# Performance work log

Hardware: AMD Instinct MI355X
Metric: run time of the kernel (lower is better)

Reference implementation:

```python
import jax, jax.numpy as jnp
import numpy as np

D_MODEL = 1024
NUM_HEADS = 16
HEAD_DIM = D_MODEL // NUM_HEADS
D_FF = 4096
BATCH = 4
SEQ = 2048
LN_EPS = 1e-6
NEG_INF = -1e10


def setup_inputs() -> dict:
    key = jax.random.key(0)
    ks = jax.random.split(key, 8)
    def lin_init(k, fan_in, fan_out):
        # flax default: lecun_normal kernel, zeros bias
        w = jax.random.normal(k, (fan_in, fan_out), jnp.float32) / np.sqrt(fan_in)
        b = jnp.zeros((fan_out,), jnp.float32)
        return w, b
    x = jax.random.normal(ks[0], (BATCH, SEQ, D_MODEL), jnp.float32)
    w_qkv, b_qkv = lin_init(ks[1], D_MODEL, 3 * D_MODEL)
    w_out, b_out = lin_init(ks[2], D_MODEL, D_MODEL)
    w_fc1, b_fc1 = lin_init(ks[3], D_MODEL, D_FF)
    w_fc2, b_fc2 = lin_init(ks[4], D_FF, D_MODEL)
    ln1_scale = jnp.ones((D_MODEL,), jnp.float32)
    ln1_bias = jnp.zeros((D_MODEL,), jnp.float32)
    ln2_scale = jnp.ones((D_MODEL,), jnp.float32)
    ln2_bias = jnp.zeros((D_MODEL,), jnp.float32)
    return {
        'x': x,
        'w_qkv': w_qkv, 'b_qkv': b_qkv,
        'w_out': w_out, 'b_out': b_out,
        'w_fc1': w_fc1, 'b_fc1': b_fc1,
        'w_fc2': w_fc2, 'b_fc2': b_fc2,
        'ln1_scale': ln1_scale, 'ln1_bias': ln1_bias,
        'ln2_scale': ln2_scale, 'ln2_bias': ln2_bias,
    }


def _layernorm(x, scale, bias):
    mu = jnp.mean(x, axis=-1, keepdims=True)
    var = jnp.mean(jnp.square(x - mu), axis=-1, keepdims=True)
    return (x - mu) * jax.lax.rsqrt(var + LN_EPS) * scale + bias


def _attention(x, w_qkv, b_qkv, w_out, b_out):
    B, S, _ = x.shape
    qkv = x @ w_qkv + b_qkv                      # [B,S,3*D]
    qkv = qkv.reshape(B, S, 3, NUM_HEADS, HEAD_DIM)
    q, k, v = qkv[:, :, 0], qkv[:, :, 1], qkv[:, :, 2]   # [B,S,H,D]
    q = q.transpose(0, 2, 1, 3)                  # [B,H,S,D]
    k = k.transpose(0, 2, 1, 3)
    v = v.transpose(0, 2, 1, 3)
    scores = jnp.einsum('bhqd,bhkd->bhqk', q, k) / np.sqrt(HEAD_DIM)
    causal = jnp.tril(jnp.ones((S, S), bool))[None, None]
    scores = jnp.where(causal, scores, NEG_INF)
    attn = jax.nn.softmax(scores, axis=-1)
    out = jnp.einsum('bhqk,bhkd->bhqd', attn, v)  # [B,H,S,D]
    out = out.transpose(0, 2, 1, 3).reshape(B, S, D_MODEL)
    return out @ w_out + b_out


def _mlp(x, w_fc1, b_fc1, w_fc2, b_fc2):
    h = jax.nn.gelu(x @ w_fc1 + b_fc1)  # approximate (tanh) gelu, matching nnx.gelu default
    return h @ w_fc2 + b_fc2


def reference(x, w_qkv, b_qkv, w_out, b_out, w_fc1, b_fc1, w_fc2, b_fc2,
              ln1_scale, ln1_bias, ln2_scale, ln2_bias):
    x = x + _attention(_layernorm(x, ln1_scale, ln1_bias), w_qkv, b_qkv, w_out, b_out)
    x = x + _mlp(_layernorm(x, ln2_scale, ln2_bias), w_fc1, b_fc1, w_fc2, b_fc2)
    return x
```

## Files before the change

### kernel.cpp

```cpp
#include <hip/hip_runtime.h>

typedef unsigned short u16;
typedef unsigned int u32;
typedef __bf16 bf16x8 __attribute__((ext_vector_type(8)));
typedef float f32x4 __attribute__((ext_vector_type(4)));

constexpr int SEQ = 2048;

__device__ __forceinline__ float bf2f(u16 u) {
    u32 x = ((u32)u) << 16;
    return __builtin_bit_cast(float, x);
}
__device__ __forceinline__ u16 f2bf(float f) {
    u32 u = __builtin_bit_cast(u32, f);
    u32 r = u + 0x7fffu + ((u >> 16) & 1u);
    return (u16)(r >> 16);
}
__device__ __forceinline__ bf16x8 ld_frag(const u16* p) {
    uint4 u = *(const uint4*)p;
    return __builtin_bit_cast(bf16x8, u);
}
__device__ __forceinline__ float gelu_f(float x) {
    float u = 0.7978845608028654f * (x + 0.044715f * x * x * x);
    float e = exp2f(u * 2.885390081777927f);
    float t = 1.f - 2.f / (1.f + e);
    return 0.5f * x * (1.f + t);
}
__device__ __forceinline__ bool probe_f32(const u32* p) { return (p[0] & 0xFFFFu) == 0u; }

__device__ __forceinline__ void load_lds16(const u16* g, u16* l) {
    __builtin_amdgcn_global_load_lds(
        (const __attribute__((address_space(1))) void*)g,
        (__attribute__((address_space(3))) void*)l, 16, 0, 0);
}

__global__ __launch_bounds__(256) void convert_to_bf16(const void* __restrict__ in, long long off,
                                                       u16* __restrict__ out, int n,
                                                       const u32* __restrict__ probe) {
    const bool f32 = probe_f32(probe);
    int i = (blockIdx.x * 256 + threadIdx.x) * 4;
    if (i >= n) return;
    if (f32) {
        const float4 v = *(const float4*)((const float*)in + off + i);
        uint2 o;
        o.x = (u32)f2bf(v.x) | ((u32)f2bf(v.y) << 16);
        o.y = (u32)f2bf(v.z) | ((u32)f2bf(v.w) << 16);
        *(uint2*)(out + i) = o;
    } else {
        *(uint2*)(out + i) = *(const uint2*)((const u16*)in + off + i);
    }
}

__global__ __launch_bounds__(256) void finalize_out(const u16* __restrict__ in, void* __restrict__ outv,
                                                    long long off, int n, const u32* __restrict__ probe) {
    const bool f32 = probe_f32(probe);
    int i = (blockIdx.x * 256 + threadIdx.x) * 4;
    if (i >= n) return;
    uint2 v = *(const uint2*)(in + i);
    if (f32) {
        float4 o;
        o.x = bf2f((u16)(v.x & 0xffffu));
        o.y = bf2f((u16)(v.x >> 16));
        o.z = bf2f((u16)(v.y & 0xffffu));
        o.w = bf2f((u16)(v.y >> 16));
        *(float4*)((float*)outv + off + i) = o;
    } else {
        *(uint2*)((u16*)outv + off + i) = v;
    }
}

__global__ __launch_bounds__(256) void transpose_any(const void* __restrict__ in,
                                                     u16* __restrict__ out,
                                                     int K, int N, const u32* __restrict__ probe) {
    const bool f32 = probe_f32(probe);
    __shared__ u16 tile[32][33];
    int tx = threadIdx.x & 31, ty = threadIdx.x >> 5;
    int k0 = blockIdx.y * 32, n0 = blockIdx.x * 32;
    for (int i = 0; i < 32; i += 8) {
        size_t idx = (size_t)(k0 + ty + i) * N + n0 + tx;
        tile[ty + i][tx] = f32 ? f2bf(((const float*)in)[idx]) : ((const u16*)in)[idx];
    }
    __syncthreads();
    for (int i = 0; i < 32; i += 8)
        out[(size_t)(n0 + ty + i) * K + k0 + tx] = tile[tx][ty + i];
}

__global__ __launch_bounds__(256) void fused_cvt_ln(const void* __restrict__ xraw, long long off,
                                                    const u16* __restrict__ sc,
                                                    const u16* __restrict__ bi,
                                                    u16* __restrict__ xbf,
                                                    u16* __restrict__ xn,
                                                    const u32* __restrict__ probe) {
    const bool f32 = probe_f32(probe);
    int row = blockIdx.x;
    int tid = threadIdx.x;
    float v[4];
    if (f32) {
        const float4 q = *(const float4*)((const float*)xraw + off + (size_t)row * 1024 + tid * 4);
        v[0] = q.x; v[1] = q.y; v[2] = q.z; v[3] = q.w;
    } else {
        uint2 u = *(const uint2*)((const u16*)xraw + off + (size_t)row * 1024 + tid * 4);
        v[0] = bf2f((u16)(u.x & 0xffffu)); v[1] = bf2f((u16)(u.x >> 16));
        v[2] = bf2f((u16)(u.y & 0xffffu)); v[3] = bf2f((u16)(u.y >> 16));
    }
    {
        uint2 c;
        c.x = (u32)f2bf(v[0]) | ((u32)f2bf(v[1]) << 16);
        c.y = (u32)f2bf(v[2]) | ((u32)f2bf(v[3]) << 16);
        *(uint2*)(xbf + (size_t)row * 1024 + tid * 4) = c;
    }
    float s1 = 0.f, s2 = 0.f;
    for (int i = 0; i < 4; i++) { s1 += v[i]; s2 += v[i] * v[i]; }
    for (int off2 = 32; off2 >= 1; off2 >>= 1) {
        s1 += __shfl_xor(s1, off2, 64);
        s2 += __shfl_xor(s2, off2, 64);
    }
    __shared__ float red[8];
    int wave = tid >> 6, lane = tid & 63;
    if (lane == 0) { red[wave] = s1; red[4 + wave] = s2; }
    __syncthreads();
    s1 = red[0] + red[1] + red[2] + red[3];
    s2 = red[4] + red[5] + red[6] + red[7];
    float mean = s1 * (1.f / 1024.f);
    float var = s2 * (1.f / 1024.f) - mean * mean;
    float rstd = rsqrtf(var + 1e-6f);
    int c = tid * 4;
    float y0 = (v[0] - mean) * rstd * bf2f(sc[c + 0]) + bf2f(bi[c + 0]);
    float y1 = (v[1] - mean) * rstd * bf2f(sc[c + 1]) + bf2f(bi[c + 1]);
    float y2 = (v[2] - mean) * rstd * bf2f(sc[c + 2]) + bf2f(bi[c + 2]);
    float y3 = (v[3] - mean) * rstd * bf2f(sc[c + 3]) + bf2f(bi[c + 3]);
    uint2 ov;
    ov.x = (u32)f2bf(y0) | ((u32)f2bf(y1) << 16);
    ov.y = (u32)f2bf(y2) | ((u32)f2bf(y3) << 16);
    *(uint2*)(xn + (size_t)row * 1024 + tid * 4) = ov;
}

__global__ __launch_bounds__(256) void layernorm_k(const u16* __restrict__ x,
                                                   const u16* __restrict__ sc,
                                                   const u16* __restrict__ bi,
                                                   u16* __restrict__ out) {
    int row = blockIdx.x;
    int tid = threadIdx.x;
    const u16* xr = x + (size_t)row * 1024;
    uint2 u = *(const uint2*)(xr + tid * 4);
    float v[4];
    v[0] = bf2f((u16)(u.x & 0xffffu));
    v[1] = bf2f((u16)(u.x >> 16));
    v[2] = bf2f((u16)(u.y & 0xffffu));
    v[3] = bf2f((u16)(u.y >> 16));
    float s1 = 0.f, s2 = 0.f;
    for (int i = 0; i < 4; i++) { s1 += v[i]; s2 += v[i] * v[i]; }
    for (int off = 32; off >= 1; off >>= 1) {
        s1 += __shfl_xor(s1, off, 64);
        s2 += __shfl_xor(s2, off, 64);
    }
    __shared__ float red[8];
    int wave = tid >> 6, lane = tid & 63;
    if (lane == 0) { red[wave] = s1; red[4 + wave] = s2; }
    __syncthreads();
    s1 = red[0] + red[1] + red[2] + red[3];
    s2 = red[4] + red[5] + red[6] + red[7];
    float mean = s1 * (1.f / 1024.f);
    float var = s2 * (1.f / 1024.f) - mean * mean;
    float rstd = rsqrtf(var + 1e-6f);
    u32 o0, o1;
    {
        int c = tid * 4;
        float y0 = (v[0] - mean) * rstd * bf2f(sc[c + 0]) + bf2f(bi[c + 0]);
        float y1 = (v[1] - mean) * rstd * bf2f(sc[c + 1]) + bf2f(bi[c + 1]);
        float y2 = (v[2] - mean) * rstd * bf2f(sc[c + 2]) + bf2f(bi[c + 2]);
        float y3 = (v[3] - mean) * rstd * bf2f(sc[c + 3]) + bf2f(bi[c + 3]);
        o0 = (u32)f2bf(y0) | ((u32)f2bf(y1) << 16);
        o1 = (u32)f2bf(y2) | ((u32)f2bf(y3) << 16);
    }
    uint2 ov; ov.x = o0; ov.y = o1;
    *(uint2*)(out + (size_t)row * 1024 + tid * 4) = ov;
}

__device__ __forceinline__ void gemm_core(const u16* __restrict__ A, const u16* __restrict__ Bt,
                                          int K, int bm, int bn,
                                          u16* lA, u16* lB, f32x4 acc[4][4]) {
    const int tid = threadIdx.x, lane = tid & 63, wave = tid >> 6;
    const int wr = (wave >> 1) * 64, wc = (wave & 1) * 64;
    const int g = lane >> 4, l15 = lane & 15;
    const int srow = wave * 32 + (lane >> 3);
    const int gslot = (lane & 7) ^ (lane >> 3);
    const u16* gA = A + (size_t)(bm + srow) * K + gslot * 8;
    const u16* gB = Bt + (size_t)(bn + srow) * K + gslot * 8;
    u16* lAb = lA + wave * 2048;
    u16* lBb = lB + wave * 2048;
    const int sw = (l15 & 7);

    for (int kk = 0; kk < K; kk += 64) {
        __syncthreads();
#pragma unroll
        for (int q = 0; q < 4; q++) {
            load_lds16(gA + kk + q * 8 * K, lAb + q * 512);
            load_lds16(gB + kk + q * 8 * K, lBb + q * 512);
        }
        __syncthreads();
#pragma unroll
        for (int kh = 0; kh < 2; kh++) {
            bf16x8 af[4], bfr[4];
#pragma unroll
            for (int i = 0; i < 4; i++)
                af[i] = ld_frag(lA + (wr + i * 16 + l15) * 64 + (((kh * 4 + g) ^ sw) * 8));
#pragma unroll
            for (int j = 0; j < 4; j++)
                bfr[j] = ld_frag(lB + (wc + j * 16 + l15) * 64 + (((kh * 4 + g) ^ sw) * 8));
#pragma unroll
            for (int i = 0; i < 4; i++)
#pragma unroll
                for (int j = 0; j < 4; j++)
                    acc[i][j] = __builtin_amdgcn_mfma_f32_16x16x32_bf16(bfr[j], af[i], acc[i][j], 0, 0, 0);
        }
    }
}

__global__ __launch_bounds__(256) void gemm_bt(const u16* __restrict__ A,
                                               const u16* __restrict__ Bt,
                                               const u16* __restrict__ bias,
                                               const u16* __restrict__ res,
                                               u16* __restrict__ out,
                                               int M, int N, int K, int epi) {
    __shared__ __align__(16) u16 lA[128 * 64];
    __shared__ __align__(16) u16 lB[128 * 64];
    const int tid = threadIdx.x, lane = tid & 63, wave = tid >> 6;
    const int wr = (wave >> 1) * 64, wc = (wave & 1) * 64;
    const int g = lane >> 4, l15 = lane & 15;
    const int bm = blockIdx.y * 128, bn = blockIdx.x * 128;

    f32x4 acc[4][4];
    f32x4 zero = {0.f, 0.f, 0.f, 0.f};
    for (int i = 0; i < 4; i++)
        for (int j = 0; j < 4; j++) acc[i][j] = zero;

    gemm_core(A, Bt, K, bm, bn, lA, lB, acc);

    for (int j = 0; j < 4; j++) {
        const int gn0 = bn + wc + j * 16 + g * 4;
        const uint2 bv2 = *(const uint2*)(bias + gn0);
        const float b0 = bf2f((u16)(bv2.x & 0xffffu)), b1 = bf2f((u16)(bv2.x >> 16));
        const float b2 = bf2f((u16)(bv2.y & 0xffffu)), b3 = bf2f((u16)(bv2.y >> 16));
        for (int i = 0; i < 4; i++) {
            const int gm = bm + wr + i * 16 + l15;
            float v0 = acc[i][j][0] + b0, v1 = acc[i][j][1] + b1;
            float v2 = acc[i][j][2] + b2, v3 = acc[i][j][3] + b3;
            if (epi == 1) {
                const uint2 rv = *(const uint2*)(res + (size_t)gm * N + gn0);
                v0 += bf2f((u16)(rv.x & 0xffffu)); v1 += bf2f((u16)(rv.x >> 16));
                v2 += bf2f((u16)(rv.y & 0xffffu)); v3 += bf2f((u16)(rv.y >> 16));
            } else if (epi == 2) {
                v0 = gelu_f(v0); v1 = gelu_f(v1); v2 = gelu_f(v2); v3 = gelu_f(v3);
            }
            ushort4 o4;
            o4.x = f2bf(v0); o4.y = f2bf(v1); o4.z = f2bf(v2); o4.w = f2bf(v3);
            *(ushort4*)(out + (size_t)gm * N + gn0) = o4;
        }
    }
}

__global__ __launch_bounds__(256) void gemm_qkv(const u16* __restrict__ A,
                                                const u16* __restrict__ Bt,
                                                const u16* __restrict__ bias,
                                                u16* __restrict__ Qg,
                                                u16* __restrict__ Kg,
                                                u16* __restrict__ VTg,
                                                int K) {
    __shared__ __align__(16) u16 lA[128 * 64];
    __shared__ __align__(16) u16 lB[128 * 64];
    const int tid = threadIdx.x, lane = tid & 63, wave = tid >> 6;
    const int wr = (wave >> 1) * 64, wc = (wave & 1) * 64;
    const int g = lane >> 4, l15 = lane & 15;
    const int bm = blockIdx.y * 128, bn = blockIdx.x * 128;
    const float QSCALE = 0.18033688011112042f;

    f32x4 acc[4][4];
    f32x4 zero = {0.f, 0.f, 0.f, 0.f};
    for (int i = 0; i < 4; i++)
        for (int j = 0; j < 4; j++) acc[i][j] = zero;

    gemm_core(A, Bt, K, bm, bn, lA, lB, acc);

    for (int j = 0; j < 4; j++) {
        const int gn0 = bn + wc + j * 16 + g * 4;
        const int which = gn0 >> 10;
        const int hh = (gn0 >> 6) & 15, d0 = gn0 & 63;
        const uint2 bv2 = *(const uint2*)(bias + gn0);
        const float b0 = bf2f((u16)(bv2.x & 0xffffu)), b1 = bf2f((u16)(bv2.x >> 16));
        const float b2 = bf2f((u16)(bv2.y & 0xffffu)), b3 = bf2f((u16)(bv2.y >> 16));
        for (int i = 0; i < 4; i++) {
            const int s0 = bm + wr + i * 16 + l15;
            const int b = s0 >> 11, srel = s0 & 2047;
            const int bh = b * 16 + hh;
            const float v0 = acc[i][j][0] + b0, v1 = acc[i][j][1] + b1;
            const float v2 = acc[i][j][2] + b2, v3 = acc[i][j][3] + b3;
            if (which == 0) {
                ushort4 o4;
                o4.x = f2bf(v0 * QSCALE); o4.y = f2bf(v1 * QSCALE);
                o4.z = f2bf(v2 * QSCALE); o4.w = f2bf(v3 * QSCALE);
                *(ushort4*)(Qg + ((size_t)bh * SEQ + srel) * 64 + d0) = o4;
            } else if (which == 1) {
                ushort4 o4;
                o4.x = f2bf(v0); o4.y = f2bf(v1); o4.z = f2bf(v2); o4.w = f2bf(v3);
                *(ushort4*)(Kg + ((size_t)bh * SEQ + srel) * 64 + d0) = o4;
            } else {
                VTg[((size_t)bh * 64 + d0 + 0) * SEQ + srel] = f2bf(v0);
                VTg[((size_t)bh * 64 + d0 + 1) * SEQ + srel] = f2bf(v1);
                VTg[((size_t)bh * 64 + d0 + 2) * SEQ + srel] = f2bf(v2);
                VTg[((size_t)bh * 64 + d0 + 3) * SEQ + srel] = f2bf(v3);
            }
        }
    }
}

__device__ __forceinline__ void stage_kv(const u16* Kbh, const u16* Vbh, int kv0,
                                         u16* bK, u16* bV, int lane, int wave) {
    const int r = lane >> 3;
    const int gs = ((lane & 7) ^ r) * 8;
#pragma unroll
    for (int q = 0; q < 2; q++) {
        const int row = q * 32 + wave * 8 + r;
        load_lds16(Kbh + (size_t)(kv0 + row) * 64 + gs, bK + q * 2048 + wave * 512 + lane * 8);
        load_lds16(Vbh + (size_t)row * SEQ + kv0 + gs, bV + q * 2048 + wave * 512 + lane * 8);
    }
}

__global__ __launch_bounds__(256) void flash_attn6(const u16* __restrict__ Qg,
                                                   const u16* __restrict__ Kg,
                                                   const u16* __restrict__ VTg,
                                                   u16* __restrict__ attn) {
    __shared__ __align__(16) u16 lK[2][64 * 64];
    __shared__ __align__(16) u16 lVt[2][64 * 64];
    __shared__ __align__(16) u16 lP[4 * 32 * 72];

    const int bh = blockIdx.y;
    const int tid = threadIdx.x, lane = tid & 63, wave = tid >> 6;
    const int g = lane >> 4, l15 = lane & 15;
    const float MASKV = -3.0e4f;

    const u16* Qbh = Qg + (size_t)bh * SEQ * 64;
    const u16* Kbh = Kg + (size_t)bh * SEQ * 64;
    const u16* Vbh = VTg + (size_t)bh * 64 * SEQ;
    u16* myP = lP + wave * 32 * 72;
    const int b = bh >> 4, h = bh & 15;
    const f32x4 zero = {0.f, 0.f, 0.f, 0.f};
    const int sw = (l15 & 7);

    for (int ph = 0; ph < 2; ph++) {
        const int ti = ph ? blockIdx.x : (15 - blockIdx.x);
        const int q0 = ti * 128;
        const int qw = q0 + wave * 32;
        const int nfull = q0 >> 6;
        const int nt = nfull + 2;

        bf16x8 qf[2][2];
#pragma unroll
        for (int mi = 0; mi < 2; mi++)
#pragma unroll
            for (int kh = 0; kh < 2; kh++)
                qf[mi][kh] = ld_frag(Qbh + (size_t)(qw + mi * 16 + l15) * 64 + kh * 32 + g * 8);

        float l_[2][4];
        f32x4 o[2][4];
        for (int mi = 0; mi < 2; mi++)
            for (int r = 0; r < 4; r++) l_[mi][r] = 0.f;
        for (int mi = 0; mi < 2; mi++)
            for (int nj = 0; nj < 4; nj++) o[mi][nj] = zero;

        __syncthreads();
        stage_kv(Kbh, Vbh, 0, lK[0], lVt[0], lane, wave);

        for (int t = 0; t < nt; t++) {
            __syncthreads();
            if (t + 1 < nt)
                stage_kv(Kbh, Vbh, (t + 1) * 64, lK[(t + 1) & 1], lVt[(t + 1) & 1], lane, wave);
            const u16* bK = lK[t & 1];
            const u16* bV = lVt[t & 1];
            const bool diag = (t >= nfull);
            const int kv0 = t * 64;

            f32x4 sc[2][4];
#pragma unroll
            for (int mi = 0; mi < 2; mi++)
                for (int nj = 0; nj < 4; nj++) sc[mi][nj] = zero;
#pragma unroll
            for (int kh = 0; kh < 2; kh++) {
                bf16x8 kf[4];
#pragma unroll
                for (int nj = 0; nj < 4; nj++)
                    kf[nj] = ld_frag(bK + (nj * 16 + l15) * 64 + (((kh * 4 + g) ^ sw) * 8));
#pragma unroll
                for (int mi = 0; mi < 2; mi++)
#pragma unroll
                    for (int nj = 0; nj < 4; nj++)
                        sc[mi][nj] = __builtin_amdgcn_mfma_f32_16x16x32_bf16(qf[mi][kh], kf[nj], sc[mi][nj], 0, 0, 0);
            }

#pragma unroll
            for (int mi = 0; mi < 2; mi++) {
#pragma unroll
                for (int r = 0; r < 4; r++) {
                    const int row = qw + mi * 16 + g * 4 + r;
                    float v0 = sc[mi][0][r], v1 = sc[mi][1][r];
                    float v2 = sc[mi][2][r], v3 = sc[mi][3][r];
                    if (diag) {
                        if (kv0 + 0 * 16 + l15 > row) v0 = MASKV;
                        if (kv0 + 1 * 16 + l15 > row) v1 = MASKV;
                        if (kv0 + 2 * 16 + l15 > row) v2 = MASKV;
                        if (kv0 + 3 * 16 + l15 > row) v3 = MASKV;
                    }
                    const float e0 = exp2f(v0), e1 = exp2f(v1);
                    const float e2 = exp2f(v2), e3 = exp2f(v3);
                    l_[mi][r] += (e0 + e1) + (e2 + e3);
                    const int prow = (mi * 16 + g * 4 + r) * 72;
                    myP[prow + 0 * 16 + l15] = f2bf(e0);
                    myP[prow + 1 * 16 + l15] = f2bf(e1);
                    myP[prow + 2 * 16 + l15] = f2bf(e2);
                    myP[prow + 3 * 16 + l15] = f2bf(e3);
                }
            }

#pragma unroll
            for (int ks = 0; ks < 2; ks++) {
                bf16x8 pa[2], vb[4];
#pragma unroll
                for (int mi = 0; mi < 2; mi++)
                    pa[mi] = ld_frag(myP + (mi * 16 + l15) * 72 + ks * 32 + g * 8);
#pragma unroll
                for (int nj = 0; nj < 4; nj++)
                    vb[nj] = ld_frag(bV + (nj * 16 + l15) * 64 + (((ks * 4 + g) ^ sw) * 8));
#pragma unroll
                for (int mi = 0; mi < 2; mi++)
#pragma unroll
                    for (int nj = 0; nj < 4; nj++)
                        o[mi][nj] = __builtin_amdgcn_mfma_f32_16x16x32_bf16(pa[mi], vb[nj], o[mi][nj], 0, 0, 0);
            }
        }

#pragma unroll
        for (int mi = 0; mi < 2; mi++) {
            for (int r = 0; r < 4; r++) {
                float ls = l_[mi][r];
                for (int off = 1; off < 16; off <<= 1) ls += __shfl_xor(ls, off, 64);
                const float inv = 1.f / ls;
                const int row = qw + mi * 16 + g * 4 + r;
                const size_t orow = ((size_t)b * SEQ + row) * 1024 + h * 64;
                for (int nj = 0; nj < 4; nj++)
                    attn[orow + nj * 16 + l15] = f2bf(o[mi][nj][r] * inv);
            }
        }
    }
}

extern "C" void kernel_launch(void* const* d_in, const int* in_sizes, int n_in,
                              void* d_out, int out_size, void* d_ws, size_t ws_size,
                              hipStream_t stream) {
    const u32* probe = (const u32*)d_in[9];
    char* ws = (char*)d_ws;
    const size_t MB = 1048576;
    auto T = [&](size_t mb) { return (u16*)(ws + mb * MB); };
    auto conv = [&](const void* src, long long off, u16* dst, int n) {
        convert_to_bf16<<<(n / 4 + 255) / 256, 256, 0, stream>>>(src, off, dst, n, probe);
    };

    if (ws_size >= 160 * MB) {
        u16* xn1 = T(0), *Qg = T(16), *Kg = T(32), *VTg = T(48), *hbuf = T(0);
        u16* attn = T(64), *xn2 = T(64), *xbf = T(80), *resid1 = T(96), *outbf = T(112);
        u16* wTq = T(128), *wTo = T(134), *wT1 = T(136), *wT2 = T(144), *vecs = T(152);
        u16 *bqkvC = vecs, *boutC = vecs + 3072, *bfc1C = vecs + 4096, *bfc2C = vecs + 8192;
        u16 *ln1sC = vecs + 9216, *ln1bC = vecs + 10240, *ln2sC = vecs + 11264, *ln2bC = vecs + 12288;
        conv(d_in[2], 0, bqkvC, 3072); conv(d_in[4], 0, boutC, 1024);
        conv(d_in[6], 0, bfc1C, 4096); conv(d_in[8], 0, bfc2C, 1024);
        conv(d_in[9], 0, ln1sC, 1024); conv(d_in[10], 0, ln1bC, 1024);
        conv(d_in[11], 0, ln2sC, 1024); conv(d_in[12], 0, ln2bC, 1024);
        transpose_any<<<dim3(96, 32), 256, 0, stream>>>(d_in[1], wTq, 1024, 3072, probe);
        transpose_any<<<dim3(32, 32), 256, 0, stream>>>(d_in[3], wTo, 1024, 1024, probe);
        transpose_any<<<dim3(128, 32), 256, 0, stream>>>(d_in[5], wT1, 1024, 4096, probe);
        transpose_any<<<dim3(32, 128), 256, 0, stream>>>(d_in[7], wT2, 4096, 1024, probe);
        fused_cvt_ln<<<8192, 256, 0, stream>>>(d_in[0], 0, ln1sC, ln1bC, xbf, xn1, probe);
        gemm_qkv<<<dim3(24, 64), 256, 0, stream>>>(xn1, wTq, bqkvC, Qg, Kg, VTg, 1024);
        flash_attn6<<<dim3(8, 64), 256, 0, stream>>>(Qg, Kg, VTg, attn);
        gemm_bt<<<dim3(8, 64), 256, 0, stream>>>(attn, wTo, boutC, xbf, resid1, 8192, 1024, 1024, 1);
        layernorm_k<<<8192, 256, 0, stream>>>(resid1, ln2sC, ln2bC, xn2);
        gemm_bt<<<dim3(32, 64), 256, 0, stream>>>(xn2, wT1, bfc1C, nullptr, hbuf, 8192, 4096, 1024, 2);
        gemm_bt<<<dim3(8, 64), 256, 0, stream>>>(hbuf, wT2, bfc2C, resid1, outbf, 8192, 1024, 4096, 1);
        finalize_out<<<8192, 256, 0, stream>>>(outbf, d_out, 0, 8388608, probe);
    } else {
        u16* vecs = T(0);
        u16 *bqkvC = vecs, *boutC = vecs + 3072, *bfc1C = vecs + 4096, *bfc2C = vecs + 8192;
        u16 *ln1sC = vecs + 9216, *ln1bC = vecs + 10240, *ln2sC = vecs + 11264, *ln2bC = vecs + 12288;
        u16* wTq = T(1), *wTo = T(7), *wT1 = T(9), *wT2 = T(17);
        u16* xbf = T(25), *xn = T(29), *Qg = T(33), *Kg = T(37), *VTg = T(41);
        u16* attn_b = T(45), *resid_b = T(49), *h_b = T(53);
        conv(d_in[2], 0, bqkvC, 3072); conv(d_in[4], 0, boutC, 1024);
        conv(d_in[6], 0, bfc1C, 4096); conv(d_in[8], 0, bfc2C, 1024);
        conv(d_in[9], 0, ln1sC, 1024); conv(d_in[10], 0, ln1bC, 1024);
        conv(d_in[11], 0, ln2sC, 1024); conv(d_in[12], 0, ln2bC, 1024);
        transpose_any<<<dim3(96, 32), 256, 0, stream>>>(d_in[1], wTq, 1024, 3072, probe);
        transpose_any<<<dim3(32, 32), 256, 0, stream>>>(d_in[3], wTo, 1024, 1024, probe);
        transpose_any<<<dim3(128, 32), 256, 0, stream>>>(d_in[5], wT1, 1024, 4096, probe);
        transpose_any<<<dim3(32, 128), 256, 0, stream>>>(d_in[7], wT2, 4096, 1024, probe);
        for (int b = 0; b < 4; b++) {
            const long long ro = (long long)b * 2048 * 1024;
            fused_cvt_ln<<<2048, 256, 0, stream>>>(d_in[0], ro, ln1sC, ln1bC, xbf, xn, probe);
            gemm_qkv<<<dim3(24, 16), 256, 0, stream>>>(xn, wTq, bqkvC, Qg, Kg, VTg, 1024);
            flash_attn6<<<dim3(8, 16), 256, 0, stream>>>(Qg, Kg, VTg, attn_b);
            gemm_bt<<<dim3(8, 16), 256, 0, stream>>>(attn_b, wTo, boutC, xbf, resid_b, 2048, 1024, 1024, 1);
            layernorm_k<<<2048, 256, 0, stream>>>(resid_b, ln2sC, ln2bC, xn);
            for (int c = 0; c < 2; c++) {
                u16* xnc = xn + (size_t)c * 1024 * 1024;
                u16* resc = resid_b + (size_t)c * 1024 * 1024;
                u16* outc = xbf + (size_t)c * 1024 * 1024;
                gemm_bt<<<dim3(32, 8), 256, 0, stream>>>(xnc, wT1, bfc1C, nullptr, h_b, 1024, 4096, 1024, 2);
                gemm_bt<<<dim3(8, 8), 256, 0, stream>>>(h_b, wT2, bfc2C, resc, outc, 1024, 1024, 4096, 1);
                finalize_out<<<1024, 256, 0, stream>>>(outc, d_out, ro + c * 1048576, 1048576, probe);
            }
        }
    }
}
```

Measured before the change: 551.9 us.

## Compute transposed attention scores so P stores pack into vector writes

Swaps the MFMA operands for the QK^T product so each lane holds four consecutive key columns for a single query row. This lets the softmax numerators be converted with the packed bf16 convert instruction and written to LDS as 8-byte stores instead of scalar 16-bit stores. Row sums are kept per lane and reduced with two cross-lane shuffles, then broadcast for normalization. The masking indices and P layout change together, so an indexing mistake would silently produce wrong results.

```diff
diff --git a/kernel.cpp b/kernel.cpp
--- a/kernel.cpp
+++ b/kernel.cpp
@@ -15,6 +15,11 @@
     u32 u = __builtin_bit_cast(u32, f);
     u32 r = u + 0x7fffu + ((u >> 16) & 1u);
     return (u16)(r >> 16);
+}
+__device__ __forceinline__ u32 cvt_pk_bf16(float a, float b) {
+    u32 d;
+    asm("v_cvt_pk_bf16_f32 %0, %1, %2" : "=v"(d) : "v"(a), "v"(b));
+    return d;
 }
 __device__ __forceinline__ bf16x8 ld_frag(const u16* p) {
     uint4 u = *(const uint4*)p;
@@ -361,10 +366,8 @@
             for (int kh = 0; kh < 2; kh++)
                 qf[mi][kh] = ld_frag(Qbh + (size_t)(qw + mi * 16 + l15) * 64 + kh * 32 + g * 8);
 
-        float l_[2][4];
+        float l_[2] = {0.f, 0.f};
         f32x4 o[2][4];
-        for (int mi = 0; mi < 2; mi++)
-            for (int r = 0; r < 4; r++) l_[mi][r] = 0.f;
         for (int mi = 0; mi < 2; mi++)
             for (int nj = 0; nj < 4; nj++) o[mi][nj] = zero;
 
@@ -380,45 +383,48 @@
             const bool diag = (t >= nfull);
             const int kv0 = t * 64;
 
-            f32x4 sc[2][4];
-#pragma unroll
-            for (int mi = 0; mi < 2; mi++)
-                for (int nj = 0; nj < 4; nj++) sc[mi][nj] = zero;
+            f32x4 sc[4][2];
+#pragma unroll
+            for (int ki = 0; ki < 4; ki++)
+                for (int mi = 0; mi < 2; mi++) sc[ki][mi] = zero;
 #pragma unroll
             for (int kh = 0; kh < 2; kh++) {
                 bf16x8 kf[4];
 #pragma unroll
-                for (int nj = 0; nj < 4; nj++)
-                    kf[nj] = ld_frag(bK + (nj * 16 + l15) * 64 + (((kh * 4 + g) ^ sw) * 8));
-#pragma unroll
-                for (int mi = 0; mi < 2; mi++)
-#pragma unroll
-                    for (int nj = 0; nj < 4; nj++)
-                        sc[mi][nj] = __builtin_amdgcn_mfma_f32_16x16x32_bf16(qf[mi][kh], kf[nj], sc[mi][nj], 0, 0, 0);
+                for (int ki = 0; ki < 4; ki++)
+                    kf[ki] = ld_frag(bK + (ki * 16 + l15) * 64 + (((kh * 4 + g) ^ sw) * 8));
+#pragma unroll
+                for (int ki = 0; ki < 4; ki++)
+#pragma unroll
+                    for (int mi = 0; mi < 2; mi++)
+                        sc[ki][mi] = __builtin_amdgcn_mfma_f32_16x16x32_bf16(kf[ki], qf[mi][kh], sc[ki][mi], 0, 0, 0);
             }
 
 #pragma unroll
             for (int mi = 0; mi < 2; mi++) {
-#pragma unroll
-                for (int r = 0; r < 4; r++) {
-                    const int row = qw + mi * 16 + g * 4 + r;
-                    float v0 = sc[mi][0][r], v1 = sc[mi][1][r];
-                    float v2 = sc[mi][2][r], v3 = sc[mi][3][r];
+                const int qrow = qw + mi * 16 + l15;
+                u16* pr = myP + (mi * 16 + l15) * 72 + g * 4;
+                float lacc = 0.f;
+#pragma unroll
+                for (int ki = 0; ki < 4; ki++) {
+                    const int kvb = kv0 + ki * 16 + g * 4;
+                    float v0 = sc[ki][mi][0], v1 = sc[ki][mi][1];
+                    float v2 = sc[ki][mi][2], v3 = sc[ki][mi][3];
                     if (diag) {
-                        if (kv0 + 0 * 16 + l15 > row) v0 = MASKV;
-                        if (kv0 + 1 * 16 + l15 > row) v1 = MASKV;
-                        if (kv0 + 2 * 16 + l15 > row) v2 = MASKV;
-                        if (kv0 + 3 * 16 + l15 > row) v3 = MASKV;
+                        if (kvb + 0 > qrow) v0 = MASKV;
+                        if (kvb + 1 > qrow) v1 = MASKV;
+                        if (kvb + 2 > qrow) v2 = MASKV;
+                        if (kvb + 3 > qrow) v3 = MASKV;
                     }
                     const float e0 = exp2f(v0), e1 = exp2f(v1);
                     const float e2 = exp2f(v2), e3 = exp2f(v3);
-                    l_[mi][r] += (e0 + e1) + (e2 + e3);
-                    const int prow = (mi * 16 + g * 4 + r) * 72;
-                    myP[prow + 0 * 16 + l15] = f2bf(e0);
-                    myP[prow + 1 * 16 + l15] = f2bf(e1);
-                    myP[prow + 2 * 16 + l15] = f2bf(e2);
-                    myP[prow + 3 * 16 + l15] = f2bf(e3);
+                    lacc += (e0 + e1) + (e2 + e3);
+                    uint2 pw;
+                    pw.x = cvt_pk_bf16(e0, e1);
+                    pw.y = cvt_pk_bf16(e2, e3);
+                    *(uint2*)(pr + ki * 16) = pw;
                 }
+                l_[mi] += lacc;
             }
 
 #pragma unroll
@@ -440,10 +446,12 @@
 
 #pragma unroll
         for (int mi = 0; mi < 2; mi++) {
+            float ls = l_[mi];
+            ls += __shfl_xor(ls, 16, 64);
+            ls += __shfl_xor(ls, 32, 64);
+#pragma unroll
             for (int r = 0; r < 4; r++) {
-                float ls = l_[mi][r];
-                for (int off = 1; off < 16; off <<= 1) ls += __shfl_xor(ls, off, 64);
-                const float inv = 1.f / ls;
+                const float inv = 1.f / __shfl(ls, g * 4 + r, 64);
                 const int row = qw + mi * 16 + g * 4 + r;
                 const size_t orow = ((size_t)b * SEQ + row) * 1024 + h * 64;
                 for (int nj = 0; nj < 4; nj++)
```

Measured after the change: 542.9 us. Within noise of the previous version (-1.6%).
